# Optimization experiments

Measured on AMD Instinct MI355X. Metric: run time of the kernel, lower is better.

## Reference

```python
import jax, jax.numpy as jnp
import numpy as np

BS, T, C, H, W = 2, 3, 256, 48, 48
NH, NP, NL = 8, 4, 3
DH = C // NH
HW = H * W
LQ = T * HW


def conv2d(x, w, b):
    # x: (N,C,H,W), w: (O,I,3,3), padding=1 (SAME)
    y = jax.lax.conv_general_dilated(x, w, (1, 1), 'SAME',
                                     dimension_numbers=('NCHW', 'OIHW', 'NCHW'))
    return y + b[None, :, None, None]


def grid_sample(img, grid, align_corners, padding_mode):
    # img: (B,C,Hi,Wi); grid: (B,Hg,Wg,2) in [-1,1], last dim = (x,y)
    B, Ch, Hi, Wi = img.shape
    gx, gy = grid[..., 0], grid[..., 1]
    if align_corners:
        x = (gx + 1.0) * 0.5 * (Wi - 1)
        y = (gy + 1.0) * 0.5 * (Hi - 1)
    else:
        x = ((gx + 1.0) * Wi - 1.0) * 0.5
        y = ((gy + 1.0) * Hi - 1.0) * 0.5
    if padding_mode == 'border':
        x = jnp.clip(x, 0.0, Wi - 1)
        y = jnp.clip(y, 0.0, Hi - 1)
    x0 = jnp.floor(x); y0 = jnp.floor(y)
    x1 = x0 + 1.0; y1 = y0 + 1.0
    wx1 = x - x0; wx0 = 1.0 - wx1
    wy1 = y - y0; wy0 = 1.0 - wy1
    imgf = img.reshape(B, Ch, Hi * Wi)

    def gather(xi, yi):
        xc = jnp.clip(xi, 0, Wi - 1).astype(jnp.int32)
        yc = jnp.clip(yi, 0, Hi - 1).astype(jnp.int32)
        flat = (yc * Wi + xc).reshape(B, 1, -1)
        g = jnp.take_along_axis(imgf, flat, axis=2).reshape(B, Ch, *xi.shape[1:])
        if padding_mode == 'zeros':
            valid = ((xi >= 0) & (xi <= Wi - 1) & (yi >= 0) & (yi <= Hi - 1))
            g = g * valid[:, None].astype(img.dtype)
        return g

    out = (gather(x0, y0) * (wx0 * wy0)[:, None]
           + gather(x1, y0) * (wx1 * wy0)[:, None]
           + gather(x0, y1) * (wx0 * wy1)[:, None]
           + gather(x1, y1) * (wx1 * wy1)[:, None])
    return out


def warp(x, flo):
    # x: (B,C,H,W), flo: (B,2,H,W) pixel flow; border padding, align_corners=True
    B, Ch, Hh, Ww = x.shape
    gy, gx = jnp.meshgrid(jnp.arange(Hh), jnp.arange(Ww), indexing='ij')
    grid = jnp.stack([gx, gy], 0).astype(x.dtype)[None]  # (1,2,H,W)
    v = grid + flo
    vx = 2.0 * v[:, 0] / max(Ww - 1, 1) - 1.0
    vy = 2.0 * v[:, 1] / max(Hh - 1, 1) - 1.0
    g = jnp.stack([vx, vy], -1)  # (B,H,W,2)
    return grid_sample(x, g, align_corners=True, padding_mode='border')


def flow_guid_offset(flow_forward, flow_backward, off, h, w):
    # off: (N, LQ, NH, NL, NP, 2) -> add frame-to-frame flows per (query level, key level)
    N = off.shape[0]
    hw = h * w
    off = off.reshape(N, NL, hw, NH, NL, NP, 2)
    f01 = flow_forward[:, 0]; f12 = flow_forward[:, 1]
    f02 = f01 + warp(f12, f01)
    b10 = flow_backward[:, 0]; b21 = flow_backward[:, 1]
    b20 = b21 + warp(b10, b21)

    def flat(f):
        return f.transpose(0, 2, 3, 1).reshape(N, hw, 2)

    f01, f12, f02, b10, b21, b20 = map(flat, (f01, f12, f02, b10, b21, b20))
    z = jnp.zeros_like(f01)
    add = jnp.stack([
        jnp.stack([z, f01, f02], axis=2),
        jnp.stack([b10, z, f12], axis=2),
        jnp.stack([b20, b21, z], axis=2)], axis=1)  # (N, 3, hw, 3, 2)
    off = off + add[:, :, :, None, :, None, :]
    return off.reshape(N, NL * hw, NH, NL, NP, 2)


def setup_inputs():
    key = jax.random.key(0)
    ks = jax.random.split(key, 12)
    query = jax.random.normal(ks[0], (BS, T, C, H, W), dtype=jnp.float32)
    input_flatten = jax.random.normal(ks[1], (BS, T, C, H, W), dtype=jnp.float32)
    reference_points = jax.random.uniform(ks[2], (BS, LQ, NL, 2), dtype=jnp.float32)
    input_spatial_shapes = jnp.array([[H, W]] * NL, dtype=jnp.int32)
    input_level_start_index = jnp.array([0, HW, 2 * HW], dtype=jnp.int32)
    input_padding_mask = jnp.zeros((BS, LQ), dtype=bool)
    flow_forward = 3.0 * jax.random.normal(ks[3], (BS, 2, 2, H, W), dtype=jnp.float32)
    flow_backward = 3.0 * jax.random.normal(ks[4], (BS, 2, 2, H, W), dtype=jnp.float32)
    # sampling_offsets bias init (as in _reset_parameters)
    thetas = np.arange(NH) * (2.0 * np.pi / NH)
    g = np.stack([np.cos(thetas), np.sin(thetas)], -1)
    g = g / np.abs(g).max(-1, keepdims=True)
    g = np.tile(g.reshape(NH, 1, 1, 2), (1, NL, NP, 1))
    g = g * (np.arange(NP) + 1).reshape(1, 1, NP, 1)
    b_off = jnp.asarray(g.reshape(-1), dtype=jnp.float32)
    fan = 1.0 / np.sqrt(C * 9)
    w_off = 0.01 * jax.random.normal(ks[5], (NH * NL * NP * 2, C, 3, 3), dtype=jnp.float32)
    w_attn = 0.01 * jax.random.normal(ks[6], (NH * NL * NP, C, 3, 3), dtype=jnp.float32)
    b_attn = jnp.zeros((NH * NL * NP,), dtype=jnp.float32)
    w_val = fan * jax.random.normal(ks[7], (C, C, 3, 3), dtype=jnp.float32)
    b_val = jnp.zeros((C,), dtype=jnp.float32)
    w_out = fan * jax.random.normal(ks[8], (C, C, 3, 3), dtype=jnp.float32)
    b_out = jnp.zeros((C,), dtype=jnp.float32)
    return {'query': query, 'reference_points': reference_points,
            'input_flatten': input_flatten,
            'input_spatial_shapes': input_spatial_shapes,
            'input_level_start_index': input_level_start_index,
            'input_padding_mask': input_padding_mask,
            'flow_forward': flow_forward, 'flow_backward': flow_backward,
            'w_off': w_off, 'b_off': b_off, 'w_attn': w_attn, 'b_attn': b_attn,
            'w_val': w_val, 'b_val': b_val, 'w_out': w_out, 'b_out': b_out}


def reference(query, reference_points, input_flatten, input_spatial_shapes,
              input_level_start_index, input_padding_mask, flow_forward,
              flow_backward, w_off, b_off, w_attn, b_attn, w_val, b_val,
              w_out, b_out):
    bs, t, c, h, w = query.shape
    q2d = query.reshape(bs * t, c, h, w)
    value = conv2d(input_flatten.reshape(bs * t, c, h, w), w_val, b_val)
    off = conv2d(q2d, w_off, b_off)
    attn = conv2d(q2d, w_attn, b_attn)

    def to_seq(x2d, ch):
        return x2d.reshape(bs, t, ch, h * w).transpose(0, 1, 3, 2).reshape(bs, t * h * w, ch)

    value = to_seq(value, c)
    off = to_seq(off, NH * NL * NP * 2)
    attn = to_seq(attn, NH * NL * NP)
    value = jnp.where(input_padding_mask[..., None], 0.0, value)
    value = value.reshape(bs, t * h * w, NH, DH)
    off = off.reshape(bs, LQ, NH, NL, NP, 2)
    off = flow_guid_offset(flow_forward, flow_backward, off, h, w)
    attn = jax.nn.softmax(attn.reshape(bs, LQ, NH, NL * NP), axis=-1)
    attn = attn.reshape(bs, LQ, NH, NL, NP)
    # offset normalizer: (W_l, H_l) per level
    norm = jnp.stack([input_spatial_shapes[:, 1], input_spatial_shapes[:, 0]], -1).astype(off.dtype)
    loc = reference_points[:, :, None, :, None, :] + off / norm[None, None, None, :, None, :]
    grids = 2.0 * loc - 1.0  # (bs, LQ, NH, NL, NP, 2)
    # values per level -> (NL*bs*NH, DH, h, w)
    v = value.reshape(bs, NL, h, w, NH, DH).transpose(1, 0, 4, 5, 2, 3).reshape(NL * bs * NH, DH, h, w)
    g = grids.transpose(3, 0, 2, 1, 4, 5).reshape(NL * bs * NH, LQ, NP, 2)
    sampled = grid_sample(v, g, align_corners=False, padding_mode='zeros')  # (NL*bs*NH, DH, LQ, NP)
    sampled = sampled.reshape(NL, bs, NH, DH, LQ, NP)
    out = jnp.einsum('lnhdqp,nqhlp->nqhd', sampled, attn).reshape(bs, LQ, c)
    out = out.reshape(bs, t, h * w, c).transpose(0, 1, 3, 2).reshape(bs * t, c, h, w)
    return conv2d(out, w_out, b_out)
```

## Files before the change

kernel.cpp:

```cpp
#include <hip/hip_runtime.h>
#include <hip/hip_bf16.h>

#define BS   2
#define T    3
#define CCH  256
#define HH   48
#define WW   48
#define NH   8
#define NP   4
#define NL   3
#define DH   32
#define HWP  (HH*WW)
#define LQ   (T*HWP)
#define NIMG (BS*T)

typedef short v8s __attribute__((ext_vector_type(8)));
typedef float v4f __attribute__((ext_vector_type(4)));
typedef float v2f __attribute__((ext_vector_type(2)));
typedef unsigned int v2u __attribute__((ext_vector_type(2)));
typedef unsigned int v4u __attribute__((ext_vector_type(4)));

__device__ __forceinline__ unsigned short f2b(float f) {
    unsigned u = __float_as_uint(f);
    return (unsigned short)((u + 0x7FFFu + ((u >> 16) & 1u)) >> 16);
}

#define GLOAD_LDS16(gp, lp) \
    __builtin_amdgcn_global_load_lds((const __attribute__((address_space(1))) unsigned int*)(const void*)(gp), \
                                     (__attribute__((address_space(3))) unsigned int*)(void*)(lp), 16, 0, 0)

#define LDS_SLAB  32768
#define LDS_ZROW  69632
#define LDS_TOTAL 69760

#define NB_FLOW 18
#define NB_WCVT 7200
#define NB_TCVT 6912
#define WS0 (9*256*256)
#define WS1 (9*288*256)

__global__ __launch_bounds__(256) void prep_kernel(
    const float* __restrict__ ff, const float* __restrict__ fb,
    float* __restrict__ addb,
    const float* __restrict__ w_val, const float* __restrict__ w_off,
    const float* __restrict__ w_attn, const float* __restrict__ w_out,
    unsigned short* __restrict__ Wb_val, unsigned short* __restrict__ Wb_oa,
    unsigned short* __restrict__ Wb_out,
    const float* __restrict__ inputf, const float* __restrict__ query,
    unsigned short* __restrict__ inb_v, unsigned short* __restrict__ inb_q)
{
    __shared__ float lds[32][33];
    const int b = blockIdx.x;
    const int tid = threadIdx.x;

    if (b < NB_FLOW) {
        int idx = b * 256 + tid;
        int n = idx / HWP, pix = idx % HWP;
        int y = pix / WW, x = pix % WW;

        auto F = [&](const float* base, int i, int c, int p) {
            return base[n * (2*2*HWP) + i * (2*HWP) + c * HWP + p];
        };

        float f01x = F(ff,0,0,pix), f01y = F(ff,0,1,pix);
        float f12x = F(ff,1,0,pix), f12y = F(ff,1,1,pix);
        float b10x = F(fb,0,0,pix), b10y = F(fb,0,1,pix);
        float b21x = F(fb,1,0,pix), b21y = F(fb,1,1,pix);

        auto bil = [&](const float* base, int i, float fx, float fy, float* ox, float* oy) {
            float vx = (float)x + fx;
            float vy = (float)y + fy;
            float gx = 2.0f * vx / (float)(WW - 1) - 1.0f;
            float gy = 2.0f * vy / (float)(HH - 1) - 1.0f;
            float px = (gx + 1.0f) * 0.5f * (float)(WW - 1);
            float py = (gy + 1.0f) * 0.5f * (float)(HH - 1);
            px = fminf(fmaxf(px, 0.0f), (float)(WW - 1));
            py = fminf(fmaxf(py, 0.0f), (float)(HH - 1));
            float x0f = floorf(px), y0f = floorf(py);
            float wx1 = px - x0f, wx0 = 1.0f - wx1;
            float wy1 = py - y0f, wy0 = 1.0f - wy1;
            int xi0 = (int)x0f, yi0 = (int)y0f;
            int xc0 = min(max(xi0, 0), WW-1), xc1 = min(max(xi0+1, 0), WW-1);
            int yc0 = min(max(yi0, 0), HH-1), yc1 = min(max(yi0+1, 0), HH-1);
            float r[2];
            #pragma unroll
            for (int c = 0; c < 2; ++c) {
                float v00 = F(base, i, c, yc0*WW + xc0);
                float v10 = F(base, i, c, yc0*WW + xc1);
                float v01 = F(base, i, c, yc1*WW + xc0);
                float v11 = F(base, i, c, yc1*WW + xc1);
                r[c] = v00*(wx0*wy0) + v10*(wx1*wy0) + v01*(wx0*wy1) + v11*(wx1*wy1);
            }
            *ox = r[0]; *oy = r[1];
        };

        float wfx, wfy; bil(ff, 1, f01x, f01y, &wfx, &wfy);
        float f02x = f01x + wfx, f02y = f01y + wfy;
        float wbx, wby; bil(fb, 0, b21x, b21y, &wbx, &wby);
        float b20x = b21x + wbx, b20y = b21y + wby;

        float* A = addb + n * (3*HWP*6) + pix * 6;
        const int TS = HWP * 6;
        A[0] = 0.f;   A[1] = 0.f;   A[2] = f01x; A[3] = f01y; A[4] = f02x; A[5] = f02y;
        A[TS+0] = b10x; A[TS+1] = b10y; A[TS+2] = 0.f; A[TS+3] = 0.f; A[TS+4] = f12x; A[TS+5] = f12y;
        A[2*TS+0] = b20x; A[2*TS+1] = b20y; A[2*TS+2] = b21x; A[2*TS+3] = b21y; A[2*TS+4] = 0.f; A[2*TS+5] = 0.f;
    } else if (b < NB_FLOW + NB_WCVT) {
        int idx = (b - NB_FLOW) * 256 + tid;
        if (idx < WS0) {
            int k = idx / (256*256), oc = (idx / 256) % 256, ic = idx % 256;
            Wb_val[idx] = f2b(w_val[((size_t)oc * 256 + ic) * 9 + k]);
        } else if (idx < WS0 + WS1) {
            int j = idx - WS0;
            int k = j / (288*256), oc = (j / 256) % 288, ic = j % 256;
            float v = (oc < 192) ? w_off[((size_t)oc * 256 + ic) * 9 + k]
                                 : w_attn[((size_t)(oc - 192) * 256 + ic) * 9 + k];
            Wb_oa[j] = f2b(v);
        } else {
            int j = idx - WS0 - WS1;
            int k = j / (256*256), oc = (j / 256) % 256, ic = j % 256;
            Wb_out[j] = f2b(w_out[((size_t)oc * 256 + ic) * 9 + k]);
        }
    } else {
        int rem = b - NB_FLOW - NB_WCVT;
        int which = rem / 3456;
        int r2 = rem % 3456;
        int px0 = (r2 % 72) * 32;
        int ic0 = ((r2 / 72) % 8) * 32;
        int img = r2 / (72 * 8);
        const float* src = which ? query : inputf;
        unsigned short* dst = which ? inb_q : inb_v;
        #pragma unroll
        for (int s = 0; s < 4; ++s) {
            int icl = (tid >> 5) + s * 8, pxl = tid & 31;
            lds[icl][pxl] = src[((size_t)img * 256 + ic0 + icl) * HWP + px0 + pxl];
        }
        __syncthreads();
        #pragma unroll
        for (int s = 0; s < 4; ++s) {
            int pxl = (tid >> 5) + s * 8, icl = tid & 31;
            dst[((size_t)img * HWP + px0 + pxl) * 256 + ic0 + icl] = f2b(lds[icl][pxl]);
        }
    }
}

template<int NM>
__device__ __forceinline__ void conv_body(
    int cls, int s, int c_lo, int c_hi,
    const char* inIc, const char* Wbc, int Mpad, int oc0, int pxb, int img,
    const float* bias_a, const float* bias_off, const float* bias_attn,
    unsigned short* Vout, float* offb, float* attnb, float* outp,
    const unsigned char* mask, char* lds)
{
    const int tid  = threadIdx.x;
    const int lane = tid & 63;
    const int wv   = tid >> 6;

    const int r0   = pxb / 48;
    const int rlo  = (r0 > 0) ? (r0 - 1) : 0;
    const int pxlo = rlo * 48;

    const int lrow8 = lane >> 3;
    const int lcol  = lane & 7;

    const int rowl = lane & 15;
    const int g    = lane >> 4;
    const int keyx = (rowl & 7) << 4;
    const int aoff0 = ((wv >> 1) * (16 * NM) + rowl) * 128;
    const int pxw   = pxb + (wv & 1) * 64;
    int ypx[4], xpx[4];
    #pragma unroll
    for (int p = 0; p < 4; ++p) {
        int px = pxw + p * 16 + rowl;
        ypx[p] = px / 48;
        xpx[p] = px % 48;
    }
    int ocr_[NM];
    #pragma unroll
    for (int j = 0; j < NM; ++j) ocr_[j] = j * 32 + wv * 8 + lrow8;

    v4f acc[NM][4];
    #pragma unroll
    for (int m = 0; m < NM; ++m)
        #pragma unroll
        for (int p = 0; p < 4; ++p)
            #pragma unroll
            for (int e = 0; e < 4; ++e) acc[m][p][e] = 0.f;

    for (int c = c_lo; c < c_hi; ++c) {
        const int ic0b = c * 128;

        #pragma unroll
        for (int rr = 0; rr < 9; ++rr) {
            int pe  = rr * 32 + wv * 8 + lrow8;
            int gpx = pxlo + pe;
            if (gpx > 2303) gpx = 2303;
            GLOAD_LDS16(inIc + (size_t)gpx * 512 + ic0b + ((lcol ^ (pe & 7)) << 4),
                        lds + LDS_SLAB + (rr * 32 + wv * 8) * 128);
        }
        #pragma unroll
        for (int j = 0; j < NM; ++j) {
            GLOAD_LDS16(Wbc + (size_t)(oc0 + ocr_[j]) * 512 + ic0b + ((lcol ^ (ocr_[j] & 7)) << 4),
                        lds + (j * 32 + wv * 8) * 128);
        }
        asm volatile("s_waitcnt vmcnt(0) lgkmcnt(0)" ::: "memory");
        __builtin_amdgcn_s_barrier();

        for (int k = 0; k < 9; ++k) {
            const int dy = k / 3 - 1, dx = k % 3 - 1;
            const int cur = k & 1;
            if (k < 8) {
                const char* wk1 = Wbc + (size_t)(k + 1) * Mpad * 512;
                #pragma unroll
                for (int j = 0; j < NM; ++j) {
                    GLOAD_LDS16(wk1 + (size_t)(oc0 + ocr_[j]) * 512 + ic0b + ((lcol ^ (ocr_[j] & 7)) << 4),
                                lds + (cur ^ 1) * 16384 + (j * 32 + wv * 8) * 128);
                }
                if (NM == 4) { asm volatile("s_waitcnt vmcnt(4)" ::: "memory"); }
                else         { asm volatile("s_waitcnt vmcnt(3)" ::: "memory"); }
            } else {
                asm volatile("s_waitcnt vmcnt(0)" ::: "memory");
            }
            __builtin_amdgcn_s_barrier();

            int bbase[4], bkey[4];
            #pragma unroll
            for (int p = 0; p < 4; ++p) {
                int ys = ypx[p] + dy, xs = xpx[p] + dx;
                bool val = ((unsigned)ys < 48u) && ((unsigned)xs < 48u);
                int pe = ys * 48 + xs - pxlo;
                bbase[p] = val ? (LDS_SLAB + pe * 128) : LDS_ZROW;
                bkey[p]  = val ? ((pe & 7) << 4) : 0;
            }

            #pragma unroll
            for (int kk = 0; kk < 2; ++kk) {
                const int col = kk * 64 + g * 16;
                v8s a[NM], bfr[4];
                #pragma unroll
                for (int m = 0; m < NM; ++m)
                    a[m] = *(const v8s*)(lds + cur * 16384 + aoff0 + m * 2048 + (col ^ keyx));
                #pragma unroll
                for (int p = 0; p < 4; ++p)
                    bfr[p] = *(const v8s*)(lds + bbase[p] + (col ^ bkey[p]));
                #pragma unroll
                for (int m = 0; m < NM; ++m)
                    #pragma unroll
                    for (int p = 0; p < 4; ++p)
                        acc[m][p] = __builtin_amdgcn_mfma_f32_16x16x32_bf16(a[m], bfr[p], acc[m][p], 0, 0, 0);
            }
            __builtin_amdgcn_s_barrier();
        }
    }

    const int n = img / T, t = img % T;
    const int ocw = oc0 + (wv >> 1) * (16 * NM);

    #pragma unroll
    for (int p = 0; p < 4; ++p) {
        const int px_f = pxw + p * 16 + rowl;
        const int q = t * HWP + px_f;
        bool mk = (cls == 0) ? (mask[n * LQ + q] != 0) : false;
        #pragma unroll
        for (int m = 0; m < NM; ++m) {
            const int oc_f = ocw + m * 16 + g * 4;
            if (cls == 0) {
                unsigned short o[4];
                #pragma unroll
                for (int r = 0; r < 4; ++r) {
                    float v = acc[m][p][r] + bias_a[oc_f + r];
                    if (mk) v = 0.f;
                    o[r] = f2b(v);
                }
                int head = oc_f >> 5, d0 = oc_f & 31;
                v2u pk;
                pk[0] = (unsigned)o[0] | ((unsigned)o[1] << 16);
                pk[1] = (unsigned)o[2] | ((unsigned)o[3] << 16);
                *(v2u*)(Vout + (((size_t)(t * BS + n) * NH + head) * HWP + px_f) * 32 + d0) = pk;
            } else if (cls == 1) {
                if (oc_f < 192) {
                    v4f v;
                    #pragma unroll
                    for (int r = 0; r < 4; ++r) v[r] = acc[m][p][r] + bias_off[oc_f + r];
                    *(v4f*)(offb + ((size_t)n * LQ + q) * 192 + oc_f) = v;
                } else {
                    v4f v;
                    #pragma unroll
                    for (int r = 0; r < 4; ++r) v[r] = acc[m][p][r] + bias_attn[oc_f - 192 + r];
                    *(v4f*)(attnb + ((size_t)n * LQ + q) * 96 + (oc_f - 192)) = v;
                }
            } else {
                #pragma unroll
                for (int r = 0; r < 4; ++r) {
                    float v = acc[m][p][r] + ((s == 0) ? bias_a[oc_f + r] : 0.f);
                    atomicAdd(&outp[((size_t)img * CCH + oc_f + r) * HWP + px_f], v);
                }
            }
        }
    }
}

__global__ __launch_bounds__(256) void convbig(
    int phase,
    const unsigned short* __restrict__ in_a,
    const unsigned short* __restrict__ in_b,
    const unsigned short* __restrict__ Wb_a,
    const unsigned short* __restrict__ Wb_b,
    const float* __restrict__ bias_a,
    const float* __restrict__ bias_off,
    const float* __restrict__ bias_attn,
    unsigned short* __restrict__ Vout,
    float* __restrict__ offb,
    float* __restrict__ attnb,
    float* __restrict__ outp,
    const unsigned char* __restrict__ mask)
{
    __shared__ __align__(16) char lds[LDS_TOTAL];

    const int tid = threadIdx.x;
    if (tid < 8) {
        v8s z;
        #pragma unroll
        for (int j = 0; j < 8; ++j) z[j] = 0;
        *(v8s*)(lds + LDS_ZROW + tid * 16) = z;
    }

    int b = blockIdx.x;
    int cls, mt, nt, img, Mpad, c_lo, c_hi, s, oc0;
    const unsigned short *inb, *Wb;
    if (phase == 0) {
        s = 0; c_lo = 0; c_hi = 4;
        if (b < 216) { cls = 0; mt = b % 2; int r = b / 2; nt = r % 18; img = r / 18;
                       inb = in_a; Wb = Wb_a; Mpad = 256; oc0 = mt * 128; }
        else { b -= 216; cls = 1; mt = b % 3; int r = b / 3; nt = r % 18; img = r / 18;
               inb = in_b; Wb = Wb_b; Mpad = 288; oc0 = mt * 96; }
    } else {
        cls = 3; s = b / 216; b = b % 216;
        c_lo = 2 * s; c_hi = c_lo + 2;
        mt = b % 2; int r = b / 2; nt = r % 18; img = r / 18;
        inb = in_a; Wb = Wb_a; Mpad = 256; oc0 = mt * 128;
    }

    const int pxb = nt * 128;
    const char* inIc = (const char*)(inb + (size_t)img * HWP * 256);
    const char* Wbc  = (const char*)Wb;

    if (cls == 1) {
        conv_body<3>(cls, s, c_lo, c_hi, inIc, Wbc, Mpad, oc0, pxb, img,
                     bias_a, bias_off, bias_attn, Vout, offb, attnb, outp, mask, lds);
    } else {
        conv_body<4>(cls, s, c_lo, c_hi, inIc, Wbc, Mpad, oc0, pxb, img,
                     bias_a, bias_off, bias_attn, Vout, offb, attnb, outp, mask, lds);
    }
}

__global__ __launch_bounds__(256) void sample_kernel(
    const unsigned short* __restrict__ V,
    const float* __restrict__ offb,
    const float* __restrict__ attnb,
    const float* __restrict__ addb,
    const float* __restrict__ refp,
    unsigned short* __restrict__ midb)
{
    const int tid = threadIdx.x;
    const int gid = tid >> 2, li = tid & 3;
    const int pair = blockIdx.x * 64 + gid;
    const int head = pair & 7;
    const int nq = pair >> 3;
    const int n = nq / LQ, q = nq % LQ;
    const int t = q / HWP, pix = q % HWP;

    const float* al = attnb + ((size_t)n * LQ + q) * 96 + head * 12;
    float lg[12];
    {
        v4f t0 = *(const v4f*)al, t1 = *(const v4f*)(al + 4), t2 = *(const v4f*)(al + 8);
        #pragma unroll
        for (int j = 0; j < 4; ++j) { lg[j] = t0[j]; lg[4+j] = t1[j]; lg[8+j] = t2[j]; }
    }
    const float* ofp = offb + ((size_t)n * LQ + q) * 192 + head * 24;
    float of[24];
    #pragma unroll
    for (int j = 0; j < 6; ++j) {
        v4f v = *(const v4f*)(ofp + j * 4);
        #pragma unroll
        for (int e = 0; e < 4; ++e) of[j*4+e] = v[e];
    }
    const float* rpp = refp + ((size_t)n * LQ + q) * 6;
    const float* adp = addb + ((size_t)n * 3 * HWP + t * HWP + pix) * 6;
    float rp[6], ad[6];
    #pragma unroll
    for (int j = 0; j < 3; ++j) {
        v2f r = *(const v2f*)(rpp + j * 2);
        v2f a = *(const v2f*)(adp + j * 2);
        rp[j*2] = r[0]; rp[j*2+1] = r[1];
        ad[j*2] = a[0]; ad[j*2+1] = a[1];
    }

    float m = lg[0];
    #pragma unroll
    for (int j = 1; j < 12; ++j) m = fmaxf(m, lg[j]);
    float s = 0.f;
    #pragma unroll
    for (int j = 0; j < 12; ++j) { lg[j] = expf(lg[j] - m); s += lg[j]; }
    float inv = 1.0f / s;
    #pragma unroll
    for (int j = 0; j < 12; ++j) lg[j] *= inv;

    float acc[8];
    #pragma unroll
    for (int e = 0; e < 8; ++e) acc[e] = 0.f;

    #pragma unroll
    for (int l = 0; l < 3; ++l) {
        float refx = rp[l*2+0], refy = rp[l*2+1];
        float addx = ad[l*2+0], addy = ad[l*2+1];
        const unsigned short* Vi =
            V + (size_t)((l * BS + n) * NH + head) * HWP * DH + li * 8;
        #pragma unroll
        for (int p = 0; p < 4; ++p) {
            float ox = of[(l*4+p)*2+0] + addx;
            float oy = of[(l*4+p)*2+1] + addy;
            float locx = refx + ox * (1.0f/48.0f);
            float locy = refy + oy * (1.0f/48.0f);
            float gx = 2.0f*locx - 1.0f;
            float gy = 2.0f*locy - 1.0f;
            float pxf = ((gx + 1.0f) * 48.0f - 1.0f) * 0.5f;
            float pyf = ((gy + 1.0f) * 48.0f - 1.0f) * 0.5f;
            float x0f = floorf(pxf), y0f = floorf(pyf);
            float wx1 = pxf - x0f, wx0 = 1.0f - wx1;
            float wy1 = pyf - y0f, wy0 = 1.0f - wy1;
            int xi0 = (int)x0f, yi0 = (int)y0f;
            bool vx0 = (x0f >= 0.0f)     && (x0f <= 47.0f);
            bool vx1 = (x0f+1.f >= 0.0f) && (x0f+1.f <= 47.0f);
            bool vy0 = (y0f >= 0.0f)     && (y0f <= 47.0f);
            bool vy1 = (y0f+1.f >= 0.0f) && (y0f+1.f <= 47.0f);
            int xc0 = min(max(xi0, 0), 47),   xc1 = min(max(xi0+1, 0), 47);
            int yc0 = min(max(yi0, 0), 47),   yc1 = min(max(yi0+1, 0), 47);
            float aw = lg[l*4+p];
            float w00 = (vx0 && vy0) ? wx0*wy0*aw : 0.f;
            float w10 = (vx1 && vy0) ? wx1*wy0*aw : 0.f;
            float w01 = (vx0 && vy1) ? wx0*wy1*aw : 0.f;
            float w11 = (vx1 && vy1) ? wx1*wy1*aw : 0.f;
            v4u u00 = *(const v4u*)(Vi + (yc0*WW + xc0)*DH);
            v4u u10 = *(const v4u*)(Vi + (yc0*WW + xc1)*DH);
            v4u u01 = *(const v4u*)(Vi + (yc1*WW + xc0)*DH);
            v4u u11 = *(const v4u*)(Vi + (yc1*WW + xc1)*DH);
            #pragma unroll
            for (int cc = 0; cc < 4; ++cc) {
                v4u u = (cc == 0) ? u00 : (cc == 1) ? u10 : (cc == 2) ? u01 : u11;
                float w = (cc == 0) ? w00 : (cc == 1) ? w10 : (cc == 2) ? w01 : w11;
                #pragma unroll
                for (int e = 0; e < 4; ++e) {
                    acc[e*2+0] += w * __uint_as_float(u[e] << 16);
                    acc[e*2+1] += w * __uint_as_float(u[e] & 0xFFFF0000u);
                }
            }
        }
    }

    v4u pk;
    #pragma unroll
    for (int e = 0; e < 4; ++e)
        pk[e] = (unsigned)f2b(acc[e*2+0]) | ((unsigned)f2b(acc[e*2+1]) << 16);
    *(v4u*)(midb + ((size_t)(n * T + t) * HWP + pix) * 256 + head * 32 + li * 8) = pk;
}

extern "C" void kernel_launch(void* const* d_in, const int* in_sizes, int n_in,
                              void* d_out, int out_size, void* d_ws, size_t ws_size,
                              hipStream_t stream) {
    const float* query  = (const float*)d_in[0];
    const float* refp   = (const float*)d_in[1];
    const float* inputf = (const float*)d_in[2];
    const unsigned char* mask = (const unsigned char*)d_in[5];
    const float* ff     = (const float*)d_in[6];
    const float* fb     = (const float*)d_in[7];
    const float* w_off  = (const float*)d_in[8];
    const float* b_off  = (const float*)d_in[9];
    const float* w_attn = (const float*)d_in[10];
    const float* b_attn = (const float*)d_in[11];
    const float* w_val  = (const float*)d_in[12];
    const float* b_val  = (const float*)d_in[13];
    const float* w_out  = (const float*)d_in[14];
    const float* b_out  = (const float*)d_in[15];

    char* w = (char*)d_ws;
    float* offb  = (float*)w;           w += (size_t)BS*LQ*192*4;
    float* attnb = (float*)w;           w += (size_t)BS*LQ*96*4;
    float* addb  = (float*)w;           w += (size_t)BS*3*HWP*6*4;
    unsigned short* V      = (unsigned short*)w; w += (size_t)48*HWP*DH*2;
    unsigned short* inb_q  = (unsigned short*)w; w += (size_t)NIMG*HWP*256*2;
    unsigned short* inb_v  = (unsigned short*)w; w += (size_t)NIMG*HWP*256*2;
    unsigned short* midb   = inb_v;
    unsigned short* Wb_val = (unsigned short*)w; w += (size_t)9*256*256*2;
    unsigned short* Wb_oa  = (unsigned short*)w; w += (size_t)9*288*256*2;
    unsigned short* Wb_out = (unsigned short*)w; w += (size_t)9*256*256*2;
    float* outp = (float*)d_out;

    hipMemsetAsync(outp, 0, (size_t)NIMG * CCH * HWP * 4, stream);

    prep_kernel<<<NB_FLOW + NB_WCVT + NB_TCVT, 256, 0, stream>>>(
        ff, fb, addb, w_val, w_off, w_attn, w_out,
        Wb_val, Wb_oa, Wb_out, inputf, query, inb_v, inb_q);

    convbig<<<540, 256, 0, stream>>>(0, inb_v, inb_q, Wb_val, Wb_oa,
                                     b_val, b_off, b_attn,
                                     V, offb, attnb, nullptr, mask);

    sample_kernel<<<(BS*LQ*NH)/64, 256, 0, stream>>>(V, offb, attnb, addb, refp, midb);

    convbig<<<432, 256, 0, stream>>>(1, midb, nullptr, Wb_out, nullptr,
                                     b_out, nullptr, nullptr,
                                     nullptr, nullptr, nullptr, outp, nullptr);
}
```

Before: 145.6 us.

## Coalesce weight conversion, swizzle conv blocks across XCDs, widen sampler per-thread channels

Weight conversion now has each thread read one (oc,ic) group's 9 contiguous taps and write them out, which cuts the block count and makes source reads contiguous. The conv kernel remaps block IDs so consecutive logical tiles land on the same XCD, aiming for better L2 reuse of shared inputs and weights. The sampler assigns 16 channels per thread instead of 8, halving the per-query offset, softmax and coordinate work at the cost of more registers and fewer threads.

```diff
diff --git a/kernel.cpp b/kernel.cpp
--- a/kernel.cpp
+++ b/kernel.cpp
@@ -33,11 +33,17 @@
 #define LDS_ZROW  69632
 #define LDS_TOTAL 69760
 
+__device__ __forceinline__ int xcd_swz(int bid, int nwg) {
+    int q = nwg >> 3, r = nwg & 7;
+    int xcd = bid & 7, j = bid >> 3;
+    return (xcd < r ? xcd * (q + 1) : r * (q + 1) + (xcd - r) * q) + j;
+}
+
 #define NB_FLOW 18
-#define NB_WCVT 7200
+#define NB_WCVT 800
 #define NB_TCVT 6912
-#define WS0 (9*256*256)
-#define WS1 (9*288*256)
+#define WP0 (256*256)
+#define WP1 (288*256)
 
 __global__ __launch_bounds__(256) void prep_kernel(
     const float* __restrict__ ff, const float* __restrict__ fb,
@@ -106,19 +112,28 @@
         A[2*TS+0] = b20x; A[2*TS+1] = b20y; A[2*TS+2] = b21x; A[2*TS+3] = b21y; A[2*TS+4] = 0.f; A[2*TS+5] = 0.f;
     } else if (b < NB_FLOW + NB_WCVT) {
         int idx = (b - NB_FLOW) * 256 + tid;
-        if (idx < WS0) {
-            int k = idx / (256*256), oc = (idx / 256) % 256, ic = idx % 256;
-            Wb_val[idx] = f2b(w_val[((size_t)oc * 256 + ic) * 9 + k]);
-        } else if (idx < WS0 + WS1) {
-            int j = idx - WS0;
-            int k = j / (288*256), oc = (j / 256) % 288, ic = j % 256;
-            float v = (oc < 192) ? w_off[((size_t)oc * 256 + ic) * 9 + k]
-                                 : w_attn[((size_t)(oc - 192) * 256 + ic) * 9 + k];
-            Wb_oa[j] = f2b(v);
+        if (idx < WP0) {
+            int oc = idx >> 8, ic = idx & 255;
+            const float* sp = w_val + ((size_t)oc * 256 + ic) * 9;
+            #pragma unroll
+            for (int j = 0; j < 9; ++j)
+                Wb_val[(size_t)j * WP0 + oc * 256 + ic] = f2b(sp[j]);
+        } else if (idx < WP0 + WP1) {
+            int p3 = idx - WP0;
+            int oc = p3 >> 8, ic = p3 & 255;
+            const float* sp = (oc < 192)
+                ? (w_off  + ((size_t)oc * 256 + ic) * 9)
+                : (w_attn + ((size_t)(oc - 192) * 256 + ic) * 9);
+            #pragma unroll
+            for (int j = 0; j < 9; ++j)
+                Wb_oa[(size_t)j * WP1 + oc * 256 + ic] = f2b(sp[j]);
         } else {
-            int j = idx - WS0 - WS1;
-            int k = j / (256*256), oc = (j / 256) % 256, ic = j % 256;
-            Wb_out[j] = f2b(w_out[((size_t)oc * 256 + ic) * 9 + k]);
+            int p3 = idx - WP0 - WP1;
+            int oc = p3 >> 8, ic = p3 & 255;
+            const float* sp = w_out + ((size_t)oc * 256 + ic) * 9;
+            #pragma unroll
+            for (int j = 0; j < 9; ++j)
+                Wb_out[(size_t)j * WP0 + oc * 256 + ic] = f2b(sp[j]);
         }
     } else {
         int rem = b - NB_FLOW - NB_WCVT;
@@ -324,7 +339,7 @@
         *(v8s*)(lds + LDS_ZROW + tid * 16) = z;
     }
 
-    int b = blockIdx.x;
+    int b = xcd_swz(blockIdx.x, gridDim.x);
     int cls, mt, nt, img, Mpad, c_lo, c_hi, s, oc0;
     const unsigned short *inb, *Wb;
     if (phase == 0) {
@@ -362,8 +377,8 @@
     unsigned short* __restrict__ midb)
 {
     const int tid = threadIdx.x;
-    const int gid = tid >> 2, li = tid & 3;
-    const int pair = blockIdx.x * 64 + gid;
+    const int gid = tid >> 1, li = tid & 1;
+    const int pair = blockIdx.x * 128 + gid;
     const int head = pair & 7;
     const int nq = pair >> 3;
     const int n = nq / LQ, q = nq % LQ;
@@ -405,16 +420,16 @@
     #pragma unroll
     for (int j = 0; j < 12; ++j) lg[j] *= inv;
 
-    float acc[8];
-    #pragma unroll
-    for (int e = 0; e < 8; ++e) acc[e] = 0.f;
+    float acc[16];
+    #pragma unroll
+    for (int e = 0; e < 16; ++e) acc[e] = 0.f;
 
     #pragma unroll
     for (int l = 0; l < 3; ++l) {
         float refx = rp[l*2+0], refy = rp[l*2+1];
         float addx = ad[l*2+0], addy = ad[l*2+1];
         const unsigned short* Vi =
-            V + (size_t)((l * BS + n) * NH + head) * HWP * DH + li * 8;
+            V + (size_t)((l * BS + n) * NH + head) * HWP * DH + li * 16;
         #pragma unroll
         for (int p = 0; p < 4; ++p) {
             float ox = of[(l*4+p)*2+0] + addx;
@@ -440,28 +455,39 @@
             float w10 = (vx1 && vy0) ? wx1*wy0*aw : 0.f;
             float w01 = (vx0 && vy1) ? wx0*wy1*aw : 0.f;
             float w11 = (vx1 && vy1) ? wx1*wy1*aw : 0.f;
-            v4u u00 = *(const v4u*)(Vi + (yc0*WW + xc0)*DH);
-            v4u u10 = *(const v4u*)(Vi + (yc0*WW + xc1)*DH);
-            v4u u01 = *(const v4u*)(Vi + (yc1*WW + xc0)*DH);
-            v4u u11 = *(const v4u*)(Vi + (yc1*WW + xc1)*DH);
-            #pragma unroll
-            for (int cc = 0; cc < 4; ++cc) {
-                v4u u = (cc == 0) ? u00 : (cc == 1) ? u10 : (cc == 2) ? u01 : u11;
-                float w = (cc == 0) ? w00 : (cc == 1) ? w10 : (cc == 2) ? w01 : w11;
-                #pragma unroll
-                for (int e = 0; e < 4; ++e) {
-                    acc[e*2+0] += w * __uint_as_float(u[e] << 16);
-                    acc[e*2+1] += w * __uint_as_float(u[e] & 0xFFFF0000u);
+            const unsigned short* p00 = Vi + (yc0*WW + xc0)*DH;
+            const unsigned short* p10 = Vi + (yc0*WW + xc1)*DH;
+            const unsigned short* p01 = Vi + (yc1*WW + xc0)*DH;
+            const unsigned short* p11 = Vi + (yc1*WW + xc1)*DH;
+            #pragma unroll
+            for (int h = 0; h < 2; ++h) {
+                v4u u00 = *(const v4u*)(p00 + h * 8);
+                v4u u10 = *(const v4u*)(p10 + h * 8);
+                v4u u01 = *(const v4u*)(p01 + h * 8);
+                v4u u11 = *(const v4u*)(p11 + h * 8);
+                #pragma unroll
+                for (int cc = 0; cc < 4; ++cc) {
+                    v4u u = (cc == 0) ? u00 : (cc == 1) ? u10 : (cc == 2) ? u01 : u11;
+                    float w = (cc == 0) ? w00 : (cc == 1) ? w10 : (cc == 2) ? w01 : w11;
+                    #pragma unroll
+                    for (int e = 0; e < 4; ++e) {
+                        acc[h*8 + e*2+0] += w * __uint_as_float(u[e] << 16);
+                        acc[h*8 + e*2+1] += w * __uint_as_float(u[e] & 0xFFFF0000u);
+                    }
                 }
             }
         }
     }
 
-    v4u pk;
-    #pragma unroll
-    for (int e = 0; e < 4; ++e)
-        pk[e] = (unsigned)f2b(acc[e*2+0]) | ((unsigned)f2b(acc[e*2+1]) << 16);
-    *(v4u*)(midb + ((size_t)(n * T + t) * HWP + pix) * 256 + head * 32 + li * 8) = pk;
+    unsigned short* mb = midb + ((size_t)(n * T + t) * HWP + pix) * 256 + head * 32 + li * 16;
+    #pragma unroll
+    for (int h = 0; h < 2; ++h) {
+        v4u pk;
+        #pragma unroll
+        for (int e = 0; e < 4; ++e)
+            pk[e] = (unsigned)f2b(acc[h*8 + e*2+0]) | ((unsigned)f2b(acc[h*8 + e*2+1]) << 16);
+        *(v4u*)(mb + h * 8) = pk;
+    }
 }
 
 extern "C" void kernel_launch(void* const* d_in, const int* in_sizes, int n_in,
@@ -505,7 +531,7 @@
                                      b_val, b_off, b_attn,
                                      V, offb, attnb, nullptr, mask);
 
-    sample_kernel<<<(BS*LQ*NH)/64, 256, 0, stream>>>(V, offb, attnb, addb, refp, midb);
+    sample_kernel<<<(BS*LQ*NH)/128, 256, 0, stream>>>(V, offb, attnb, addb, refp, midb);
 
     convbig<<<432, 256, 0, stream>>>(1, midb, nullptr, Wb_out, nullptr,
                                      b_out, nullptr, nullptr,
```

New measurement: 196.7 us. +35.1%, slower.
